# Kernel tuning notes

Measured on AMD Instinct MI355X. Metric: run time of the kernel, lower is better.

Reference implementation:

```python
import jax, jax.numpy as jnp
import numpy as np

VOCAB = 256
PAD = 0
D_MODEL = 512
ATTN_DIM = 64
B, L = 8, 2048
LN_EPS = 1e-5


def layer_norm(x, g, b):
    mu = jnp.mean(x, axis=-1, keepdims=True)
    var = jnp.mean(jnp.square(x - mu), axis=-1, keepdims=True)
    return (x - mu) * jax.lax.rsqrt(var + LN_EPS) * g + b


def setup_inputs() -> dict:
    key = jax.random.key(0)
    ks = jax.random.split(key, 10)
    tokens = jax.random.randint(ks[0], (B, L), 1, VOCAB)  # avoid PAD=0
    prefix_lens = jax.random.randint(ks[1], (B,), 256, 1536)
    embed_w = jax.random.normal(ks[2], (VOCAB, D_MODEL), jnp.float32) * 0.02
    embed_w = embed_w.at[PAD].set(0.0)  # padding_idx row
    en_g = jnp.ones((D_MODEL,), jnp.float32)
    en_b = jnp.zeros((D_MODEL,), jnp.float32)
    fn_g = jnp.ones((D_MODEL,), jnp.float32)
    fn_b = jnp.zeros((D_MODEL,), jnp.float32)
    q_w = jax.random.normal(ks[3], (ATTN_DIM, D_MODEL), jnp.float32) * 0.02
    q_b = jnp.zeros((ATTN_DIM,), jnp.float32)
    k_w = jax.random.normal(ks[4], (ATTN_DIM, D_MODEL), jnp.float32) * 0.02
    k_b = jnp.zeros((ATTN_DIM,), jnp.float32)
    g_w = jax.random.normal(ks[5], (1, D_MODEL), jnp.float32) * 0.02
    g_b = jnp.full((1,), 2.0, jnp.float32)  # gate bias init to 2.0
    return dict(tokens=tokens, prefix_lens=prefix_lens, embed_w=embed_w,
                en_g=en_g, en_b=en_b, fn_g=fn_g, fn_b=fn_b,
                q_w=q_w, q_b=q_b, k_w=k_w, k_b=k_b, g_w=g_w, g_b=g_b)


def reference(tokens, prefix_lens, embed_w, en_g, en_b, fn_g, fn_b,
              q_w, q_b, k_w, k_b, g_w, g_b):
    # encode (n_layers=0: embed -> embed_norm -> final_norm)
    x = embed_w[tokens]                       # (B, L, D)
    x = layer_norm(x, en_g, en_b)
    h = layer_norm(x, fn_g, fn_b)

    vocab_logits = jnp.einsum('bld,vd->blv', h, embed_w)   # tied head
    q = h @ q_w.T + q_b                       # (B, L, A)
    k = h @ k_w.T + k_b                       # (B, L, A)
    scores = jnp.einsum('btd,bsd->bts', q, k) / np.sqrt(ATTN_DIM).astype(np.float32)

    idx = jnp.arange(L)[None, :]              # (1, L)
    prefix_mask = (idx < prefix_lens[:, None]) & (tokens != PAD)  # (B, L)
    scores = jnp.where(prefix_mask[:, None, :], scores, -jnp.inf)
    attn = jax.nn.softmax(scores, axis=-1)    # (B, L, L)

    prefix_onehot = jax.nn.one_hot(tokens, VOCAB, dtype=jnp.float32)
    prefix_onehot = prefix_onehot * prefix_mask[..., None]
    copy_dist = jnp.einsum('bts,bsv->btv', attn, prefix_onehot)  # (B, L, V)

    gate = jax.nn.sigmoid(h @ g_w.T + g_b)    # (B, L, 1)
    vocab_probs = jax.nn.softmax(vocab_logits, axis=-1)
    mixed = gate * vocab_probs + (1.0 - gate) * copy_dist
    mixed = jnp.clip(mixed, 1e-12, None)
    return jnp.log(mixed), gate[..., 0], attn
```

## Files before the change

kernel.cpp:

```cpp
#include <hip/hip_runtime.h>
#include <math.h>


#define DM 512
#define VC 256
#define SL 2048
#define NB 8
#define AD 64

typedef float f4v __attribute__((ext_vector_type(4)));

__device__ __forceinline__ float wave_sum(float v) {
#pragma unroll
  for (int o = 32; o > 0; o >>= 1) v += __shfl_xor(v, o, 64);
  return v;
}
__device__ __forceinline__ float wave_max(float v) {
#pragma unroll
  for (int o = 32; o > 0; o >>= 1) v = fmaxf(v, __shfl_xor(v, o, 64));
  return v;
}
__device__ __forceinline__ float blk_sum(float v, float* red) {
  v = wave_sum(v);
  if ((threadIdx.x & 63) == 0) red[threadIdx.x >> 6] = v;
  __syncthreads();
  float r = red[0] + red[1] + red[2] + red[3];
  __syncthreads();
  return r;
}
__device__ __forceinline__ float blk_max(float v, float* red) {
  v = wave_max(v);
  if ((threadIdx.x & 63) == 0) red[threadIdx.x >> 6] = v;
  __syncthreads();
  float r = fmaxf(fmaxf(red[0], red[1]), fmaxf(red[2], red[3]));
  __syncthreads();
  return r;
}

__global__ __launch_bounds__(256) void kprep(
    const float* __restrict__ embed_w, const float* __restrict__ q_w,
    const float* __restrict__ k_w, const int* __restrict__ tokens,
    const int* __restrict__ prefix_lens,
    float* __restrict__ embed_P, float* __restrict__ qk_P,
    int* __restrict__ cnt)
{
  __shared__ int c[VC];
  const int blk = blockIdx.x;
  const int tid = threadIdx.x;
  if (blk < DM) {
    const int d = blk;
    embed_P[(((d >> 2) * VC + tid) << 2) + (d & 3)] = embed_w[tid * DM + d];
    if (tid < 128) {
      float val = (tid < 64) ? q_w[tid * DM + d] : k_w[(tid - 64) * DM + d];
      qk_P[(((d >> 2) * 128 + tid) << 2) + (d & 3)] = val;
    }
  } else {
    const int b = blk - DM;
    c[tid] = 0;
    __syncthreads();
    const int P = prefix_lens[b];
    for (int s = tid; s < SL; s += 256) {
      if (s < P) {
        int t = tokens[b * SL + s];
        if (t != 0) atomicAdd(&c[t], 1);
      }
    }
    __syncthreads();
    cnt[b * VC + tid] = c[tid];
  }
}

__global__ __launch_bounds__(256) void ktok(
    const float* __restrict__ embed_w,
    const float* __restrict__ en_g, const float* __restrict__ en_b,
    const float* __restrict__ fn_g, const float* __restrict__ fn_b,
    const float* __restrict__ q_b, const float* __restrict__ k_b,
    const float* __restrict__ g_w, const float* __restrict__ g_b,
    const float* __restrict__ embed_P, const float* __restrict__ qk_P,
    float* __restrict__ q_tok, float* __restrict__ kT_P,
    float* __restrict__ gate_tok, float* __restrict__ probs_tok)
{
  __shared__ float red[4];
  __shared__ __align__(16) float hs[DM];
  const int tt = blockIdx.x;
  const int tid = threadIdx.x;

  float x0 = embed_w[tt * DM + tid];
  float x1 = embed_w[tt * DM + 256 + tid];
  float mu = blk_sum(x0 + x1, red) * (1.0f / DM);
  float d0 = x0 - mu, d1 = x1 - mu;
  float var = blk_sum(d0 * d0 + d1 * d1, red) * (1.0f / DM);
  float inv = 1.0f / sqrtf(var + 1e-5f);
  float y0 = d0 * inv * en_g[tid] + en_b[tid];
  float y1 = d1 * inv * en_g[tid + 256] + en_b[tid + 256];
  mu = blk_sum(y0 + y1, red) * (1.0f / DM);
  d0 = y0 - mu; d1 = y1 - mu;
  var = blk_sum(d0 * d0 + d1 * d1, red) * (1.0f / DM);
  inv = 1.0f / sqrtf(var + 1e-5f);
  float h0 = d0 * inv * fn_g[tid] + fn_b[tid];
  float h1 = d1 * inv * fn_g[tid + 256] + fn_b[tid + 256];
  hs[tid] = h0; hs[tid + 256] = h1;
  float gp = blk_sum(h0 * g_w[tid] + h1 * g_w[tid + 256], red);
  if (tid == 0) gate_tok[tt] = 1.0f / (1.0f + expf(-(gp + g_b[0])));

  const float4* hs4 = (const float4*)hs;
  if (tid < 128) {
    const float4* w4p = (const float4*)qk_P;
    float acc = 0.0f;
#pragma unroll 8
    for (int d4 = 0; d4 < DM / 4; ++d4) {
      float4 h4 = hs4[d4];
      float4 w4 = w4p[d4 * 128 + tid];
      acc += h4.x * w4.x + h4.y * w4.y + h4.z * w4.z + h4.w * w4.w;
    }
    if (tid < 64) {
      q_tok[tt * AD + tid] = acc + q_b[tid];
    } else {
      int a = tid - 64;
      kT_P[(((a >> 2) * VC + tt) << 2) + (a & 3)] = acc + k_b[a];
    }
  }
  const float4* e4p = (const float4*)embed_P;
  float lt = 0.0f;
#pragma unroll 8
  for (int d4 = 0; d4 < DM / 4; ++d4) {
    float4 h4 = hs4[d4];
    float4 e4 = e4p[d4 * VC + tid];
    lt += h4.x * e4.x + h4.y * e4.y + h4.z * e4.z + h4.w * e4.w;
  }
  float m = blk_max(lt, red);
  float e = expf(lt - m);
  float Z = blk_sum(e, red);
  probs_tok[tt * VC + tid] = e / Z;
}

__global__ __launch_bounds__(256) void ktables(
    const float* __restrict__ q_tok, const float* __restrict__ kT_P,
    const int* __restrict__ cnt, const float* __restrict__ gate_tok,
    const float* __restrict__ probs_tok,
    float* __restrict__ e_norm, float* __restrict__ logmix)
{
  __shared__ float red[4];
  __shared__ __align__(16) float qs[AD];
  const int b = blockIdx.x >> 8, tt = blockIdx.x & 255;
  const int v = threadIdx.x;
  if (v < AD) qs[v] = q_tok[tt * AD + v];
  __syncthreads();
  const float4* qs4 = (const float4*)qs;
  const float4* k4p = (const float4*)kT_P;
  float sv = 0.0f;
#pragma unroll
  for (int a4 = 0; a4 < AD / 4; ++a4) {
    float4 q4 = qs4[a4];
    float4 k4 = k4p[a4 * VC + v];
    sv += q4.x * k4.x + q4.y * k4.y + q4.z * k4.z + q4.w * k4.w;
  }
  sv *= 0.125f;
  int c = cnt[b * VC + v];
  float m = blk_max(c > 0 ? sv : -1e30f, red);
  float e = expf(sv - m);
  float Z = blk_sum((float)c * e, red);
  float en = e / Z;
  int idx = (b * VC + tt) * VC + v;
  e_norm[idx] = en;
  float g = gate_tok[tt];
  float mixed = g * probs_tok[tt * VC + v] + (1.0f - g) * ((float)c * en);
  logmix[idx] = logf(fmaxf(mixed, 1e-12f));
}

__global__ __launch_bounds__(256) void kwrite(
    const int* __restrict__ tokens, const int* __restrict__ prefix_lens,
    const float* __restrict__ e_norm, const float* __restrict__ logmix,
    const float* __restrict__ gate_tok,
    float* __restrict__ out_logmix, float* __restrict__ out_gate,
    float* __restrict__ out_attn)
{
  __shared__ float erow[VC];
  const int row = blockIdx.x;
  const int b = row >> 11;
  const int tid = threadIdx.x;
  const int tt = tokens[row];
  const int base = (b * VC + tt) * VC;
  erow[tid] = e_norm[base + tid];
  out_logmix[(size_t)row * VC + tid] = logmix[base + tid];
  if (tid == 0) out_gate[row] = gate_tok[tt];
  const int P = prefix_lens[b];
  __syncthreads();
  const int4* tokrow = (const int4*)(tokens + b * SL);
  f4v* arow = (f4v*)(out_attn + (size_t)row * SL);
#pragma unroll
  for (int it = 0; it < 2; ++it) {
    int i = tid + it * 256;
    int4 tk = tokrow[i];
    int s0 = i * 4;
    f4v val;
    val.x = (s0     < P && tk.x != 0) ? erow[tk.x] : 0.0f;
    val.y = (s0 + 1 < P && tk.y != 0) ? erow[tk.y] : 0.0f;
    val.z = (s0 + 2 < P && tk.z != 0) ? erow[tk.z] : 0.0f;
    val.w = (s0 + 3 < P && tk.w != 0) ? erow[tk.w] : 0.0f;
    __builtin_nontemporal_store(val, &arow[i]);
  }
}

extern "C" void kernel_launch(void* const* d_in, const int* in_sizes, int n_in,
                              void* d_out, int out_size, void* d_ws, size_t ws_size,
                              hipStream_t stream)
{
  const int*   tokens      = (const int*)  d_in[0];
  const int*   prefix_lens = (const int*)  d_in[1];
  const float* embed_w     = (const float*)d_in[2];
  const float* en_g        = (const float*)d_in[3];
  const float* en_b        = (const float*)d_in[4];
  const float* fn_g        = (const float*)d_in[5];
  const float* fn_b        = (const float*)d_in[6];
  const float* q_b         = (const float*)d_in[8];
  const float* k_b         = (const float*)d_in[10];
  const float* q_w         = (const float*)d_in[7];
  const float* k_w         = (const float*)d_in[9];
  const float* g_w         = (const float*)d_in[11];
  const float* g_b         = (const float*)d_in[12];

  float* ws        = (float*)d_ws;
  float* embed_P   = ws;
  float* qk_P      = embed_P + DM * VC;
  float* kT_P      = qk_P + DM * 128;
  float* q_tok     = kT_P + AD * VC;
  float* gate_tok  = q_tok + VC * AD;
  float* probs_tok = gate_tok + VC;
  int*   cnt       = (int*)(probs_tok + VC * VC);
  float* e_norm    = (float*)(cnt + NB * VC);
  float* logmix    = e_norm + NB * VC * VC;

  float* out_logmix = (float*)d_out;
  float* out_gate   = out_logmix + (size_t)NB * SL * VC;
  float* out_attn   = out_gate + (size_t)NB * SL;

  kprep<<<DM + NB, 256, 0, stream>>>(embed_w, q_w, k_w, tokens, prefix_lens,
                                     embed_P, qk_P, cnt);
  ktok<<<VC, 256, 0, stream>>>(embed_w, en_g, en_b, fn_g, fn_b, q_b, k_b,
                               g_w, g_b, embed_P, qk_P,
                               q_tok, kT_P, gate_tok, probs_tok);
  ktables<<<NB * VC, 256, 0, stream>>>(q_tok, kT_P, cnt, gate_tok, probs_tok,
                                       e_norm, logmix);
  kwrite<<<NB * SL, 256, 0, stream>>>(tokens, prefix_lens, e_norm, logmix,
                                      gate_tok, out_logmix, out_gate, out_attn);
}
```

Before: 217.9 us.

## Precompute per-(batch,token) attention rows then copy them into output

Adds a kernel that builds the full attention row once for each (batch, token-id) pair into a workspace table of 8×256×2048 floats (16 MB). The write kernel then copies the matching precomputed row instead of doing a gather from shared memory for every sequence position. This removes repeated gather and mask work per output row. The cost is an extra 16 MB write plus reads that may be served from cache, and an extra kernel launch.

```diff
diff --git a/kernel.cpp b/kernel.cpp
--- a/kernel.cpp
+++ b/kernel.cpp
@@ -168,26 +168,18 @@
   logmix[idx] = logf(fmaxf(mixed, 1e-12f));
 }
 
-__global__ __launch_bounds__(256) void kwrite(
+__global__ __launch_bounds__(256) void kbuild(
     const int* __restrict__ tokens, const int* __restrict__ prefix_lens,
-    const float* __restrict__ e_norm, const float* __restrict__ logmix,
-    const float* __restrict__ gate_tok,
-    float* __restrict__ out_logmix, float* __restrict__ out_gate,
-    float* __restrict__ out_attn)
+    const float* __restrict__ e_norm, float* __restrict__ A)
 {
   __shared__ float erow[VC];
-  const int row = blockIdx.x;
-  const int b = row >> 11;
-  const int tid = threadIdx.x;
-  const int tt = tokens[row];
-  const int base = (b * VC + tt) * VC;
-  erow[tid] = e_norm[base + tid];
-  out_logmix[(size_t)row * VC + tid] = logmix[base + tid];
-  if (tid == 0) out_gate[row] = gate_tok[tt];
+  const int b = blockIdx.x >> 8, tt = blockIdx.x & 255;
+  const int tid = threadIdx.x;
+  erow[tid] = e_norm[(b * VC + tt) * VC + tid];
   const int P = prefix_lens[b];
   __syncthreads();
   const int4* tokrow = (const int4*)(tokens + b * SL);
-  f4v* arow = (f4v*)(out_attn + (size_t)row * SL);
+  f4v* arow = (f4v*)(A + ((size_t)(b * VC + tt)) * SL);
 #pragma unroll
   for (int it = 0; it < 2; ++it) {
     int i = tid + it * 256;
@@ -198,7 +190,30 @@
     val.y = (s0 + 1 < P && tk.y != 0) ? erow[tk.y] : 0.0f;
     val.z = (s0 + 2 < P && tk.z != 0) ? erow[tk.z] : 0.0f;
     val.w = (s0 + 3 < P && tk.w != 0) ? erow[tk.w] : 0.0f;
-    __builtin_nontemporal_store(val, &arow[i]);
+    arow[i] = val;
+  }
+}
+
+__global__ __launch_bounds__(256) void kwrite(
+    const int* __restrict__ tokens,
+    const float* __restrict__ A, const float* __restrict__ logmix,
+    const float* __restrict__ gate_tok,
+    float* __restrict__ out_logmix, float* __restrict__ out_gate,
+    float* __restrict__ out_attn)
+{
+  const int row = blockIdx.x;
+  const int b = row >> 11;
+  const int tid = threadIdx.x;
+  const int tt = tokens[row];
+  out_logmix[(size_t)row * VC + tid] = logmix[(b * VC + tt) * VC + tid];
+  if (tid == 0) out_gate[row] = gate_tok[tt];
+  const f4v* src = (const f4v*)(A + ((size_t)(b * VC + tt)) * SL);
+  f4v* dst = (f4v*)(out_attn + (size_t)row * SL);
+#pragma unroll
+  for (int it = 0; it < 2; ++it) {
+    int i = tid + it * 256;
+    f4v v = src[i];
+    __builtin_nontemporal_store(v, &dst[i]);
   }
 }
 
@@ -213,10 +228,10 @@
   const float* en_b        = (const float*)d_in[4];
   const float* fn_g        = (const float*)d_in[5];
   const float* fn_b        = (const float*)d_in[6];
+  const float* q_w         = (const float*)d_in[7];
   const float* q_b         = (const float*)d_in[8];
+  const float* k_w         = (const float*)d_in[9];
   const float* k_b         = (const float*)d_in[10];
-  const float* q_w         = (const float*)d_in[7];
-  const float* k_w         = (const float*)d_in[9];
   const float* g_w         = (const float*)d_in[11];
   const float* g_b         = (const float*)d_in[12];
 
@@ -230,6 +245,7 @@
   int*   cnt       = (int*)(probs_tok + VC * VC);
   float* e_norm    = (float*)(cnt + NB * VC);
   float* logmix    = e_norm + NB * VC * VC;
+  float* A         = logmix + NB * VC * VC;
 
   float* out_logmix = (float*)d_out;
   float* out_gate   = out_logmix + (size_t)NB * SL * VC;
@@ -242,6 +258,7 @@
                                q_tok, kT_P, gate_tok, probs_tok);
   ktables<<<NB * VC, 256, 0, stream>>>(q_tok, kT_P, cnt, gate_tok, probs_tok,
                                        e_norm, logmix);
-  kwrite<<<NB * SL, 256, 0, stream>>>(tokens, prefix_lens, e_norm, logmix,
-                                      gate_tok, out_logmix, out_gate, out_attn);
-}
+  kbuild<<<NB * VC, 256, 0, stream>>>(tokens, prefix_lens, e_norm, A);
+  kwrite<<<NB * SL, 256, 0, stream>>>(tokens, A, logmix, gate_tok,
+                                      out_logmix, out_gate, out_attn);
+}
```

New measurement: 225.4 us. 1.03x slower.

## Process eight output rows per block in kwrite with shared token row

Applied to the files above, without the earlier changes.

The write kernel now handles eight consecutive query rows per block instead of one. It stages the batch's token row in shared memory once and reuses it across the rows. The PAD check is folded into setting erows[r][0] to zero, and the logmix copy now uses nontemporal stores. This cuts block count and repeated token loads, at the cost of more shared memory per block and fewer blocks in flight for a write-bound kernel.

```diff
diff --git a/kernel.cpp b/kernel.cpp
--- a/kernel.cpp
+++ b/kernel.cpp
@@ -7,6 +7,7 @@
 #define SL 2048
 #define NB 8
 #define AD 64
+#define G 8
 
 typedef float f4v __attribute__((ext_vector_type(4)));
 
@@ -175,30 +176,49 @@
     float* __restrict__ out_logmix, float* __restrict__ out_gate,
     float* __restrict__ out_attn)
 {
-  __shared__ float erow[VC];
-  const int row = blockIdx.x;
-  const int b = row >> 11;
+  __shared__ float erows[G][VC];
+  __shared__ int4 tok4[SL / 4];
+  __shared__ int tts[G];
+  const int blk = blockIdx.x;
+  const int b = blk >> 8;
+  const int r0 = (blk & 255) * G;
+  const int row0 = b * SL + r0;
   const int tid = threadIdx.x;
-  const int tt = tokens[row];
-  const int base = (b * VC + tt) * VC;
-  erow[tid] = e_norm[base + tid];
-  out_logmix[(size_t)row * VC + tid] = logmix[base + tid];
-  if (tid == 0) out_gate[row] = gate_tok[tt];
+
+  if (tid < G) tts[tid] = tokens[row0 + tid];
+  const int4* tokrow = (const int4*)(tokens + b * SL);
+  tok4[tid] = tokrow[tid];
+  tok4[tid + 256] = tokrow[tid + 256];
+  __syncthreads();
+
+#pragma unroll
+  for (int r = 0; r < G; ++r) {
+    int tt = tts[r];
+    float ev = e_norm[(b * VC + tt) * VC + tid];
+    erows[r][tid] = (tid == 0) ? 0.0f : ev;
+    __builtin_nontemporal_store(logmix[(b * VC + tt) * VC + tid],
+                                &out_logmix[(size_t)(row0 + r) * VC + tid]);
+  }
+  if (tid < G) out_gate[row0 + tid] = gate_tok[tts[tid]];
   const int P = prefix_lens[b];
   __syncthreads();
-  const int4* tokrow = (const int4*)(tokens + b * SL);
-  f4v* arow = (f4v*)(out_attn + (size_t)row * SL);
+
 #pragma unroll
   for (int it = 0; it < 2; ++it) {
     int i = tid + it * 256;
-    int4 tk = tokrow[i];
+    int4 tk = tok4[i];
     int s0 = i * 4;
-    f4v val;
-    val.x = (s0     < P && tk.x != 0) ? erow[tk.x] : 0.0f;
-    val.y = (s0 + 1 < P && tk.y != 0) ? erow[tk.y] : 0.0f;
-    val.z = (s0 + 2 < P && tk.z != 0) ? erow[tk.z] : 0.0f;
-    val.w = (s0 + 3 < P && tk.w != 0) ? erow[tk.w] : 0.0f;
-    __builtin_nontemporal_store(val, &arow[i]);
+    bool m0 = s0 < P, m1 = s0 + 1 < P, m2 = s0 + 2 < P, m3 = s0 + 3 < P;
+#pragma unroll
+    for (int r = 0; r < G; ++r) {
+      f4v val;
+      val.x = m0 ? erows[r][tk.x] : 0.0f;
+      val.y = m1 ? erows[r][tk.y] : 0.0f;
+      val.z = m2 ? erows[r][tk.z] : 0.0f;
+      val.w = m3 ? erows[r][tk.w] : 0.0f;
+      f4v* dst = (f4v*)(out_attn + (size_t)(row0 + r) * SL);
+      __builtin_nontemporal_store(val, &dst[i]);
+    }
   }
 }
 
@@ -213,10 +233,10 @@
   const float* en_b        = (const float*)d_in[4];
   const float* fn_g        = (const float*)d_in[5];
   const float* fn_b        = (const float*)d_in[6];
+  const float* q_w         = (const float*)d_in[7];
   const float* q_b         = (const float*)d_in[8];
+  const float* k_w         = (const float*)d_in[9];
   const float* k_b         = (const float*)d_in[10];
-  const float* q_w         = (const float*)d_in[7];
-  const float* k_w         = (const float*)d_in[9];
   const float* g_w         = (const float*)d_in[11];
   const float* g_b         = (const float*)d_in[12];
 
@@ -242,6 +262,7 @@
                                q_tok, kT_P, gate_tok, probs_tok);
   ktables<<<NB * VC, 256, 0, stream>>>(q_tok, kT_P, cnt, gate_tok, probs_tok,
                                        e_norm, logmix);
-  kwrite<<<NB * SL, 256, 0, stream>>>(tokens, prefix_lens, e_norm, logmix,
-                                      gate_tok, out_logmix, out_gate, out_attn);
-}
+  kwrite<<<NB * SL / G, 256, 0, stream>>>(tokens, prefix_lens, e_norm, logmix,
+                                          gate_tok, out_logmix, out_gate,
+                                          out_attn);
+}
```

Result: no change. 218.3 us (+0.2%).
